# Kernel tuning notes

Measured on AMD Instinct MI355X. Metric: run time of the kernel, lower is better.

The kernel has to match this reference:

```python
import jax, jax.numpy as jnp
import numpy as np

FP8_MAX = 448.0  # torch.finfo(float8_e4m3fn).max

def _fp8_round(v):
    # round-to-nearest fp8 e4m3fn, back to f32 (simulated quantization)
    return v.astype(jnp.float8_e4m3fn).astype(jnp.float32)

def setup_inputs() -> dict:
    key = jax.random.key(0)
    k_x, k_w, k_b = jax.random.split(key, 3)
    M, K, N = 8, 8192, 8192
    x = jax.random.normal(k_x, (M, K), dtype=jnp.float32)
    w = jax.random.normal(k_w, (K, N), dtype=jnp.float32) * 0.02
    # per-output-column weight quantization (amax-to-scale)
    w_amax = jnp.max(jnp.abs(w), axis=0)                      # [N]
    w_scale = jnp.where(w_amax > 0, FP8_MAX / w_amax, 1.0)    # [N]
    weight_fp8_t = _fp8_round(w * w_scale[None, :])           # [K, N] fp8 values in f32
    weight_scale_inv = (1.0 / w_scale).astype(jnp.float32)    # [N]
    bias = jax.random.normal(k_b, (N,), dtype=jnp.float32) * 0.01
    return {"x": x, "weight_fp8_t": weight_fp8_t,
            "weight_scale_inv": weight_scale_inv, "bias": bias}

def reference(x, weight_fp8_t, weight_scale_inv, bias):
    # dynamic per-row activation quantization: amax -> scale
    amax = jnp.max(jnp.abs(x), axis=-1)                       # [M]
    x_scale = jnp.where(amax > 0, FP8_MAX / amax, 1.0)        # [M]
    x_fp8 = _fp8_round(x * x_scale[:, None])                  # [M, K]
    # scaled matmul: acc * x_scale_inv * weight_scale_inv (per row / per col)
    acc = jnp.einsum('mk,kn->mn', x_fp8, weight_fp8_t)        # [M, N]
    y = acc * (1.0 / x_scale)[:, None] * weight_scale_inv[None, :]
    return y + bias[None, :]
```

## Files before the change

### kernel.cpp

```cpp
#include <hip/hip_runtime.h>
#include <stdint.h>

#define MM 8
#define KK 8192
#define NN 8192
#define KC 256
#define FP8MAXV 448.0f

__device__ __forceinline__ float fp8_e4m3_round(float v) {
    uint32_t u = __float_as_uint(v);
    uint32_t mag = u & 0x7fffffffu;
    if (mag >= 0x3C800000u) {
        uint32_t lsb = (u >> 20) & 1u;
        uint32_t r = u + 0x0007FFFFu + lsb;
        r &= 0xFFF00000u;
        return __uint_as_float(r);
    }
    return rintf(v * 512.0f) * (1.0f / 512.0f);
}

__global__ __launch_bounds__(256) void prep_kernel(const float* __restrict__ x,
                                                   float* __restrict__ ws) {
    const int m = blockIdx.x;
    const int tid = threadIdx.x;
    const float* row = x + (size_t)m * KK;

    float amax = 0.0f;
    for (int k = tid * 4; k < KK; k += 256 * 4) {
        float4 v = *(const float4*)(row + k);
        amax = fmaxf(amax, fmaxf(fmaxf(fabsf(v.x), fabsf(v.y)),
                                 fmaxf(fabsf(v.z), fabsf(v.w))));
    }
#pragma unroll
    for (int off = 32; off >= 1; off >>= 1)
        amax = fmaxf(amax, __shfl_xor(amax, off, 64));

    __shared__ float sred[4];
    __shared__ float sscale;
    if ((tid & 63) == 0) sred[tid >> 6] = amax;
    __syncthreads();
    if (tid == 0) {
        float a = fmaxf(fmaxf(sred[0], sred[1]), fmaxf(sred[2], sred[3]));
        float scale = (a > 0.0f) ? (FP8MAXV / a) : 1.0f;
        sscale = scale;
        ws[m] = 1.0f / scale;
    }
    __syncthreads();
    const float scale = sscale;

    float* xqT = ws + 64;
    for (int k = tid; k < KK; k += 256)
        xqT[(size_t)k * MM + m] = fp8_e4m3_round(row[k] * scale);
}

__global__ __launch_bounds__(256) void init_kernel(const float* __restrict__ bias,
                                                   float* __restrict__ out) {
    int idx = blockIdx.x * 256 + threadIdx.x;
    out[idx] = bias[idx & (NN - 1)];
}

__global__ __launch_bounds__(256) void gemm_kernel(const float* __restrict__ W,
                                                   const float* __restrict__ wsinv,
                                                   const float* __restrict__ ws,
                                                   float* __restrict__ out) {
    const int n  = blockIdx.x * 256 + threadIdx.x;
    const int k0 = blockIdx.y * KC;

    __shared__ float sxq[KC * MM];
    {
        const float4* src = (const float4*)(ws + 64 + (size_t)k0 * MM);
        float4* dst = (float4*)sxq;
#pragma unroll
        for (int i = 0; i < (KC * MM) / 4 / 256; ++i)
            dst[threadIdx.x + i * 256] = src[threadIdx.x + i * 256];
    }
    __syncthreads();

    float acc[MM];
#pragma unroll
    for (int m = 0; m < MM; ++m) acc[m] = 0.0f;

    const float* Wp = W + (size_t)k0 * NN + n;
#pragma unroll 8
    for (int k = 0; k < KC; ++k) {
        float w = Wp[(size_t)k * NN];
        const float4* a4 = (const float4*)(sxq + k * MM);
        float4 a0 = a4[0];
        float4 a1 = a4[1];
        acc[0] = fmaf(a0.x, w, acc[0]);
        acc[1] = fmaf(a0.y, w, acc[1]);
        acc[2] = fmaf(a0.z, w, acc[2]);
        acc[3] = fmaf(a0.w, w, acc[3]);
        acc[4] = fmaf(a1.x, w, acc[4]);
        acc[5] = fmaf(a1.y, w, acc[5]);
        acc[6] = fmaf(a1.z, w, acc[6]);
        acc[7] = fmaf(a1.w, w, acc[7]);
    }

    const float wsn = wsinv[n];
#pragma unroll
    for (int m = 0; m < MM; ++m)
        unsafeAtomicAdd(out + (size_t)m * NN + n, acc[m] * ws[m] * wsn);
}

extern "C" void kernel_launch(void* const* d_in, const int* in_sizes, int n_in,
                              void* d_out, int out_size, void* d_ws, size_t ws_size,
                              hipStream_t stream) {
    const float* x     = (const float*)d_in[0];
    const float* W     = (const float*)d_in[1];
    const float* wsinv = (const float*)d_in[2];
    const float* bias  = (const float*)d_in[3];
    float* out = (float*)d_out;
    float* ws  = (float*)d_ws;

    prep_kernel<<<MM, 256, 0, stream>>>(x, ws);
    init_kernel<<<(MM * NN) / 256, 256, 0, stream>>>(bias, out);
    gemm_kernel<<<dim3(NN / 256, KK / KC), 256, 0, stream>>>(W, wsinv, ws, out);
}
```

Measured before the change: 63.63 us.

## Vectorize GEMM to four columns per thread and fuse prep with bias init

Each GEMM thread now handles four adjacent output columns using 16-byte nontemporal weight loads, with KC halved to 128 so the grid stays large enough. The prep and bias-init kernels are merged into one launch to save a kernel dispatch. The changes target per-load instruction overhead on the 256MB f32 weight stream and launch overhead. In exchange each thread holds 32 accumulators, and twice as many K-chunks issue scalar atomics into the output.

```diff
diff --git a/kernel.cpp b/kernel.cpp
--- a/kernel.cpp
+++ b/kernel.cpp
@@ -4,8 +4,10 @@
 #define MM 8
 #define KK 8192
 #define NN 8192
-#define KC 256
+#define KC 128
 #define FP8MAXV 448.0f
+
+typedef float f32x4 __attribute__((ext_vector_type(4)));
 
 __device__ __forceinline__ float fp8_e4m3_round(float v) {
     uint32_t u = __float_as_uint(v);
@@ -19,15 +21,22 @@
     return rintf(v * 512.0f) * (1.0f / 512.0f);
 }
 
-__global__ __launch_bounds__(256) void prep_kernel(const float* __restrict__ x,
-                                                   float* __restrict__ ws) {
+__global__ __launch_bounds__(256) void prep_init_kernel(const float* __restrict__ x,
+                                                        const float* __restrict__ bias,
+                                                        float* __restrict__ ws,
+                                                        float* __restrict__ out) {
+    if (blockIdx.x >= MM) {
+        int idx = (blockIdx.x - MM) * 256 + threadIdx.x;
+        out[idx] = bias[idx & (NN - 1)];
+        return;
+    }
     const int m = blockIdx.x;
     const int tid = threadIdx.x;
     const float* row = x + (size_t)m * KK;
 
     float amax = 0.0f;
     for (int k = tid * 4; k < KK; k += 256 * 4) {
-        float4 v = *(const float4*)(row + k);
+        f32x4 v = *(const f32x4*)(row + k);
         amax = fmaxf(amax, fmaxf(fmaxf(fabsf(v.x), fabsf(v.y)),
                                  fmaxf(fabsf(v.z), fabsf(v.w))));
     }
@@ -53,54 +62,49 @@
         xqT[(size_t)k * MM + m] = fp8_e4m3_round(row[k] * scale);
 }
 
-__global__ __launch_bounds__(256) void init_kernel(const float* __restrict__ bias,
-                                                   float* __restrict__ out) {
-    int idx = blockIdx.x * 256 + threadIdx.x;
-    out[idx] = bias[idx & (NN - 1)];
-}
-
 __global__ __launch_bounds__(256) void gemm_kernel(const float* __restrict__ W,
                                                    const float* __restrict__ wsinv,
                                                    const float* __restrict__ ws,
                                                    float* __restrict__ out) {
-    const int n  = blockIdx.x * 256 + threadIdx.x;
+    const int n4 = (blockIdx.x * 256 + threadIdx.x) * 4;
     const int k0 = blockIdx.y * KC;
 
     __shared__ float sxq[KC * MM];
-    {
-        const float4* src = (const float4*)(ws + 64 + (size_t)k0 * MM);
-        float4* dst = (float4*)sxq;
-#pragma unroll
-        for (int i = 0; i < (KC * MM) / 4 / 256; ++i)
-            dst[threadIdx.x + i * 256] = src[threadIdx.x + i * 256];
-    }
+    ((f32x4*)sxq)[threadIdx.x] =
+        ((const f32x4*)(ws + 64 + (size_t)k0 * MM))[threadIdx.x];
     __syncthreads();
 
-    float acc[MM];
+    f32x4 acc[MM];
 #pragma unroll
-    for (int m = 0; m < MM; ++m) acc[m] = 0.0f;
+    for (int m = 0; m < MM; ++m) acc[m] = (f32x4)0.0f;
 
-    const float* Wp = W + (size_t)k0 * NN + n;
+    const float* Wp = W + (size_t)k0 * NN + n4;
 #pragma unroll 8
     for (int k = 0; k < KC; ++k) {
-        float w = Wp[(size_t)k * NN];
-        const float4* a4 = (const float4*)(sxq + k * MM);
-        float4 a0 = a4[0];
-        float4 a1 = a4[1];
-        acc[0] = fmaf(a0.x, w, acc[0]);
-        acc[1] = fmaf(a0.y, w, acc[1]);
-        acc[2] = fmaf(a0.z, w, acc[2]);
-        acc[3] = fmaf(a0.w, w, acc[3]);
-        acc[4] = fmaf(a1.x, w, acc[4]);
-        acc[5] = fmaf(a1.y, w, acc[5]);
-        acc[6] = fmaf(a1.z, w, acc[6]);
-        acc[7] = fmaf(a1.w, w, acc[7]);
+        f32x4 w = __builtin_nontemporal_load((const f32x4*)(Wp + (size_t)k * NN));
+        const f32x4* a4 = (const f32x4*)(sxq + k * MM);
+        f32x4 a0 = a4[0];
+        f32x4 a1 = a4[1];
+        acc[0] += w * a0.x;
+        acc[1] += w * a0.y;
+        acc[2] += w * a0.z;
+        acc[3] += w * a0.w;
+        acc[4] += w * a1.x;
+        acc[5] += w * a1.y;
+        acc[6] += w * a1.z;
+        acc[7] += w * a1.w;
     }
 
-    const float wsn = wsinv[n];
+    const f32x4 wsn = *(const f32x4*)(wsinv + n4);
 #pragma unroll
-    for (int m = 0; m < MM; ++m)
-        unsafeAtomicAdd(out + (size_t)m * NN + n, acc[m] * ws[m] * wsn);
+    for (int m = 0; m < MM; ++m) {
+        f32x4 r = acc[m] * (ws[m] * wsn);
+        float* o = out + (size_t)m * NN + n4;
+        unsafeAtomicAdd(o + 0, r.x);
+        unsafeAtomicAdd(o + 1, r.y);
+        unsafeAtomicAdd(o + 2, r.z);
+        unsafeAtomicAdd(o + 3, r.w);
+    }
 }
 
 extern "C" void kernel_launch(void* const* d_in, const int* in_sizes, int n_in,
@@ -113,7 +117,6 @@
     float* out = (float*)d_out;
     float* ws  = (float*)d_ws;
 
-    prep_kernel<<<MM, 256, 0, stream>>>(x, ws);
-    init_kernel<<<(MM * NN) / 256, 256, 0, stream>>>(bias, out);
-    gemm_kernel<<<dim3(NN / 256, KK / KC), 256, 0, stream>>>(W, wsinv, ws, out);
+    prep_init_kernel<<<MM + (MM * NN) / 256, 256, 0, stream>>>(x, bias, ws, out);
+    gemm_kernel<<<dim3(NN / 1024, KK / KC), 256, 0, stream>>>(W, wsinv, ws, out);
 }
```

Result: slower. 134.5 us (+111.4%).

## Replace split-K atomics with partial-sum buffer plus separate reduction kernel

Applied to the files above, without the earlier changes.

The split-K GEMM now writes per-chunk partial results to a workspace buffer, and a separate reduction kernel sums the 32 partials with the bias. The atomic path is kept as a fallback when the workspace is too small. The accumulators use 2-wide float vectors, which may map to packed FMA instructions, and launch bounds now request 4 blocks per SM. This removes atomic contention on the output but adds about 8 MB of partial-sum writes and reads plus an extra launch.

```diff
diff --git a/kernel.cpp b/kernel.cpp
--- a/kernel.cpp
+++ b/kernel.cpp
@@ -5,7 +5,14 @@
 #define KK 8192
 #define NN 8192
 #define KC 256
+#define KSPLIT (KK / KC)
 #define FP8MAXV 448.0f
+
+typedef float f32x4 __attribute__((ext_vector_type(4)));
+typedef float f32x2 __attribute__((ext_vector_type(2)));
+
+#define XQT_OFF 64
+#define PART_OFF (XQT_OFF + KK * MM)
 
 __device__ __forceinline__ float fp8_e4m3_round(float v) {
     uint32_t u = __float_as_uint(v);
@@ -27,7 +34,7 @@
 
     float amax = 0.0f;
     for (int k = tid * 4; k < KK; k += 256 * 4) {
-        float4 v = *(const float4*)(row + k);
+        f32x4 v = *(const f32x4*)(row + k);
         amax = fmaxf(amax, fmaxf(fmaxf(fabsf(v.x), fabsf(v.y)),
                                  fmaxf(fabsf(v.z), fabsf(v.w))));
     }
@@ -48,9 +55,60 @@
     __syncthreads();
     const float scale = sscale;
 
-    float* xqT = ws + 64;
+    float* xqT = ws + XQT_OFF;
     for (int k = tid; k < KK; k += 256)
         xqT[(size_t)k * MM + m] = fp8_e4m3_round(row[k] * scale);
+}
+
+__global__ __launch_bounds__(256, 4) void gemm_partial(const float* __restrict__ W,
+                                                       const float* __restrict__ wsinv,
+                                                       const float* __restrict__ ws,
+                                                       float* __restrict__ part) {
+    const int n  = blockIdx.x * 256 + threadIdx.x;
+    const int c  = blockIdx.y;
+    const int k0 = c * KC;
+
+    __shared__ float sxq[KC * MM];
+    {
+        const f32x4* src = (const f32x4*)(ws + XQT_OFF + (size_t)k0 * MM);
+        ((f32x4*)sxq)[threadIdx.x]       = src[threadIdx.x];
+        ((f32x4*)sxq)[threadIdx.x + 256] = src[threadIdx.x + 256];
+    }
+    __syncthreads();
+
+    f32x2 acc[4];
+#pragma unroll
+    for (int i = 0; i < 4; ++i) acc[i] = (f32x2)0.0f;
+
+    const float* Wp = W + (size_t)k0 * NN + n;
+#pragma unroll 8
+    for (int k = 0; k < KC; ++k) {
+        float w = Wp[(size_t)k * NN];
+        const f32x2* a2 = (const f32x2*)(sxq + k * MM);
+        acc[0] += a2[0] * w;
+        acc[1] += a2[1] * w;
+        acc[2] += a2[2] * w;
+        acc[3] += a2[3] * w;
+    }
+
+    const float wsn = wsinv[n];
+    float* p = part + ((size_t)c * MM) * NN + n;
+#pragma unroll
+    for (int i = 0; i < 4; ++i) {
+        p[(size_t)(2 * i + 0) * NN] = acc[i].x * (ws[2 * i + 0] * wsn);
+        p[(size_t)(2 * i + 1) * NN] = acc[i].y * (ws[2 * i + 1] * wsn);
+    }
+}
+
+__global__ __launch_bounds__(256) void reduce_kernel(const float* __restrict__ part,
+                                                     const float* __restrict__ bias,
+                                                     float* __restrict__ out) {
+    const int idx = blockIdx.x * 256 + threadIdx.x;
+    float s = bias[idx & (NN - 1)];
+#pragma unroll
+    for (int c = 0; c < KSPLIT; ++c)
+        s += part[(size_t)c * MM * NN + idx];
+    out[idx] = s;
 }
 
 __global__ __launch_bounds__(256) void init_kernel(const float* __restrict__ bias,
@@ -59,48 +117,42 @@
     out[idx] = bias[idx & (NN - 1)];
 }
 
-__global__ __launch_bounds__(256) void gemm_kernel(const float* __restrict__ W,
-                                                   const float* __restrict__ wsinv,
-                                                   const float* __restrict__ ws,
-                                                   float* __restrict__ out) {
+__global__ __launch_bounds__(256, 4) void gemm_atomic(const float* __restrict__ W,
+                                                      const float* __restrict__ wsinv,
+                                                      const float* __restrict__ ws,
+                                                      float* __restrict__ out) {
     const int n  = blockIdx.x * 256 + threadIdx.x;
     const int k0 = blockIdx.y * KC;
 
     __shared__ float sxq[KC * MM];
     {
-        const float4* src = (const float4*)(ws + 64 + (size_t)k0 * MM);
-        float4* dst = (float4*)sxq;
-#pragma unroll
-        for (int i = 0; i < (KC * MM) / 4 / 256; ++i)
-            dst[threadIdx.x + i * 256] = src[threadIdx.x + i * 256];
+        const f32x4* src = (const f32x4*)(ws + XQT_OFF + (size_t)k0 * MM);
+        ((f32x4*)sxq)[threadIdx.x]       = src[threadIdx.x];
+        ((f32x4*)sxq)[threadIdx.x + 256] = src[threadIdx.x + 256];
     }
     __syncthreads();
 
-    float acc[MM];
+    f32x2 acc[4];
 #pragma unroll
-    for (int m = 0; m < MM; ++m) acc[m] = 0.0f;
+    for (int i = 0; i < 4; ++i) acc[i] = (f32x2)0.0f;
 
     const float* Wp = W + (size_t)k0 * NN + n;
 #pragma unroll 8
     for (int k = 0; k < KC; ++k) {
         float w = Wp[(size_t)k * NN];
-        const float4* a4 = (const float4*)(sxq + k * MM);
-        float4 a0 = a4[0];
-        float4 a1 = a4[1];
-        acc[0] = fmaf(a0.x, w, acc[0]);
-        acc[1] = fmaf(a0.y, w, acc[1]);
-        acc[2] = fmaf(a0.z, w, acc[2]);
-        acc[3] = fmaf(a0.w, w, acc[3]);
-        acc[4] = fmaf(a1.x, w, acc[4]);
-        acc[5] = fmaf(a1.y, w, acc[5]);
-        acc[6] = fmaf(a1.z, w, acc[6]);
-        acc[7] = fmaf(a1.w, w, acc[7]);
+        const f32x2* a2 = (const f32x2*)(sxq + k * MM);
+        acc[0] += a2[0] * w;
+        acc[1] += a2[1] * w;
+        acc[2] += a2[2] * w;
+        acc[3] += a2[3] * w;
     }
 
     const float wsn = wsinv[n];
 #pragma unroll
-    for (int m = 0; m < MM; ++m)
-        unsafeAtomicAdd(out + (size_t)m * NN + n, acc[m] * ws[m] * wsn);
+    for (int i = 0; i < 4; ++i) {
+        unsafeAtomicAdd(out + (size_t)(2 * i + 0) * NN + n, acc[i].x * (ws[2 * i + 0] * wsn));
+        unsafeAtomicAdd(out + (size_t)(2 * i + 1) * NN + n, acc[i].y * (ws[2 * i + 1] * wsn));
+    }
 }
 
 extern "C" void kernel_launch(void* const* d_in, const int* in_sizes, int n_in,
@@ -113,7 +165,16 @@
     float* out = (float*)d_out;
     float* ws  = (float*)d_ws;
 
+    const size_t need = (size_t)(PART_OFF + (size_t)KSPLIT * MM * NN) * sizeof(float);
+
     prep_kernel<<<MM, 256, 0, stream>>>(x, ws);
-    init_kernel<<<(MM * NN) / 256, 256, 0, stream>>>(bias, out);
-    gemm_kernel<<<dim3(NN / 256, KK / KC), 256, 0, stream>>>(W, wsinv, ws, out);
+
+    if (ws_size >= need) {
+        float* part = ws + PART_OFF;
+        gemm_partial<<<dim3(NN / 256, KSPLIT), 256, 0, stream>>>(W, wsinv, ws, part);
+        reduce_kernel<<<(MM * NN) / 256, 256, 0, stream>>>(part, bias, out);
+    } else {
+        init_kernel<<<(MM * NN) / 256, 256, 0, stream>>>(bias, out);
+        gemm_atomic<<<dim3(NN / 256, KSPLIT), 256, 0, stream>>>(W, wsinv, ws, out);
+    }
 }
```

After: 65.23 us. +2.5%, slower.
